# Performance work log

Hardware: AMD Instinct MI355X
Metric: run time of the kernel (lower is better)

## Reference

```python
import jax, jax.numpy as jnp
import numpy as np

B, N, C, H = 2, 2048, 768, 12
HD = C // H  # head dim = 64


def setup_inputs() -> dict:
    key = jax.random.key(0)
    k1, k2, k3 = jax.random.split(key, 3)
    x = jax.random.normal(k1, (B, N, C), dtype=jnp.float32)
    w_qkv = jax.random.normal(k2, (C, 3 * C), dtype=jnp.float32) * (C ** -0.5)
    w_proj = jax.random.normal(k3, (C, C), dtype=jnp.float32) * (C ** -0.5)
    b_proj = jnp.zeros((C,), dtype=jnp.float32)
    return {"x": x, "w_qkv": w_qkv, "w_proj": w_proj, "b_proj": b_proj}


def reference(x, w_qkv, w_proj, b_proj):
    scale = HD ** -0.5
    # qkv projection: [B,N,3C] -> [3,B,H,N,HD]
    qkv = (x @ w_qkv).reshape(B, N, 3, H, HD).transpose(2, 0, 3, 1, 4)
    q, k, v = qkv[0], qkv[1], qkv[2]
    # explicit QK^T softmax V (materializes [B,H,N,N] scores, as in source)
    attn = jnp.einsum("bhqd,bhkd->bhqk", q, k) * scale
    attn = jax.nn.softmax(attn, axis=-1)
    out = jnp.einsum("bhqk,bhkd->bhqd", attn, v)
    out = out.transpose(0, 2, 1, 3).reshape(B, N, C)
    return out @ w_proj + b_proj
```

## Files before the change

kernel.cpp:

```cpp
#include <hip/hip_runtime.h>

#define C_DIM 768
#define NSEQ 2048
#define H_DIM 12
#define HD 64
#define M_ROWS 4096
#define KSPLIT 4

typedef float f32x4 __attribute__((ext_vector_type(4)));
typedef short bf16x8 __attribute__((ext_vector_type(8)));
typedef _Float16 f16x8 __attribute__((ext_vector_type(8)));
typedef _Float16 f16x4 __attribute__((ext_vector_type(4)));
typedef __fp16 fp16x2 __attribute__((ext_vector_type(2)));
typedef __fp16 fp16x4 __attribute__((ext_vector_type(4)));
typedef unsigned short u16;

#define MFMA_PV(a, b, c) __builtin_amdgcn_mfma_f32_16x16x16f16(a, b, c, 0, 0, 0)

typedef unsigned int __attribute__((address_space(1))) as1_uint;
typedef unsigned int __attribute__((address_space(3))) as3_uint;
__device__ __forceinline__ void dma16(const void* g, void* l) {
  __builtin_amdgcn_global_load_lds((const as1_uint*)g, (as3_uint*)l, 16, 0, 0);
}

__device__ __forceinline__ u16 f2bf(float f) {
  union { float f; unsigned u; } v; v.f = f;
  unsigned u = v.u + 0x7FFFu + ((v.u >> 16) & 1u);
  return (u16)(u >> 16);
}

__global__ __launch_bounds__(256) void prep_kernel(const float* __restrict__ x,
                                                   const float* __restrict__ wq,
                                                   const float* __restrict__ wp,
                                                   u16* __restrict__ x_bf,
                                                   u16* __restrict__ outq,
                                                   u16* __restrict__ outp) {
  if (blockIdx.z == 2) {
    const int n4 = M_ROWS * C_DIM / 4;
    int lb = blockIdx.y * 72 + blockIdx.x;
    int i0 = lb * 256 + threadIdx.x;
    {
      float4 v = ((const float4*)x)[i0];
      ushort4 o;
      o.x = f2bf(v.x); o.y = f2bf(v.y); o.z = f2bf(v.z); o.w = f2bf(v.w);
      ((ushort4*)x_bf)[i0] = o;
    }
    int i1 = i0 + 442368;
    if (i1 < n4) {
      float4 v = ((const float4*)x)[i1];
      ushort4 o;
      o.x = f2bf(v.x); o.y = f2bf(v.y); o.z = f2bf(v.z); o.w = f2bf(v.w);
      ((ushort4*)x_bf)[i1] = o;
    }
    return;
  }
  const float* in; u16* out; int Cc;
  if (blockIdx.z == 0) { in = wq; out = outq; Cc = 3 * C_DIM; }
  else { if (blockIdx.x >= 24) return; in = wp; out = outp; Cc = C_DIM; }
  const int R = C_DIM;
  __shared__ float t[32][33];
  int tx = threadIdx.x & 31, ty = threadIdx.x >> 5;
  int c0 = blockIdx.x * 32, r0 = blockIdx.y * 32;
#pragma unroll
  for (int i = 0; i < 4; i++)
    t[ty + i * 8][tx] = in[(size_t)(r0 + ty + i * 8) * Cc + c0 + tx];
  __syncthreads();
#pragma unroll
  for (int i = 0; i < 4; i++)
    out[(size_t)(c0 + ty + i * 8) * R + r0 + tx] = f2bf(t[tx][ty + i * 8]);
}

__device__ __forceinline__ void gemm_core_128(const u16* __restrict__ A,
                                              const u16* __restrict__ BT,
                                              int m0, int n0,
                                              u16* la, u16* lb, f32x4 acc[4][4]) {
  const int K = C_DIM;
  int tid = threadIdx.x, lane = tid & 63, wave = tid >> 6;
  int wm = (wave >> 1) * 64, wn = (wave & 1) * 64;
  int quad = lane >> 4, l16 = lane & 15;

  int r0 = wave * 16 + (lane >> 2);
  int sw = (((lane & 3) ^ (r0 & 3)) * 8);
  const u16* ga0 = A + (size_t)(m0 + r0) * K + sw;
  const u16* ga1 = A + (size_t)(m0 + r0 + 64) * K + sw;
  const u16* gb0 = BT + (size_t)(n0 + r0) * K + sw;
  const u16* gb1 = BT + (size_t)(n0 + r0 + 64) * K + sw;
  u16* lA0 = la + wave * 16 * 32;
  u16* lA1 = lA0 + 64 * 32;
  u16* lB0 = lb + wave * 16 * 32;
  u16* lB1 = lB0 + 64 * 32;

  for (int k0 = 0; k0 < K; k0 += 32) {
    __syncthreads();
    dma16(ga0 + k0, lA0);
    dma16(ga1 + k0, lA1);
    dma16(gb0 + k0, lB0);
    dma16(gb1 + k0, lB1);
    __syncthreads();
    bf16x8 af[4], bfr[4];
#pragma unroll
    for (int mt = 0; mt < 4; mt++) {
      int r = wm + mt * 16 + l16;
      af[mt] = *(const bf16x8*)(la + r * 32 + ((quad ^ (r & 3)) * 8));
    }
#pragma unroll
    for (int nt = 0; nt < 4; nt++) {
      int r = wn + nt * 16 + l16;
      bfr[nt] = *(const bf16x8*)(lb + r * 32 + ((quad ^ (r & 3)) * 8));
    }
#pragma unroll
    for (int mt = 0; mt < 4; mt++)
#pragma unroll
      for (int nt = 0; nt < 4; nt++)
        acc[mt][nt] = __builtin_amdgcn_mfma_f32_16x16x32_bf16(af[mt], bfr[nt], acc[mt][nt], 0, 0, 0);
  }
}

__device__ __forceinline__ void gemm_core_64(const u16* __restrict__ A,
                                             const u16* __restrict__ BT,
                                             int m0, int n0,
                                             u16* la, u16* lb, f32x4 acc[2][4]) {
  const int K = C_DIM;
  int tid = threadIdx.x, lane = tid & 63, wave = tid >> 6;
  int wm = (wave >> 1) * 32, wn = (wave & 1) * 64;
  int quad = lane >> 4, l16 = lane & 15;

  int r0 = wave * 16 + (lane >> 2);
  int sw = (((lane & 3) ^ (r0 & 3)) * 8);
  const u16* ga0 = A + (size_t)(m0 + r0) * K + sw;
  const u16* gb0 = BT + (size_t)(n0 + r0) * K + sw;
  const u16* gb1 = BT + (size_t)(n0 + r0 + 64) * K + sw;
  u16* lA0 = la + wave * 16 * 32;
  u16* lB0 = lb + wave * 16 * 32;
  u16* lB1 = lB0 + 64 * 32;

  for (int k0 = 0; k0 < K; k0 += 32) {
    __syncthreads();
    dma16(ga0 + k0, lA0);
    dma16(gb0 + k0, lB0);
    dma16(gb1 + k0, lB1);
    __syncthreads();
    bf16x8 af[2], bfr[4];
#pragma unroll
    for (int mt = 0; mt < 2; mt++) {
      int r = wm + mt * 16 + l16;
      af[mt] = *(const bf16x8*)(la + r * 32 + ((quad ^ (r & 3)) * 8));
    }
#pragma unroll
    for (int nt = 0; nt < 4; nt++) {
      int r = wn + nt * 16 + l16;
      bfr[nt] = *(const bf16x8*)(lb + r * 32 + ((quad ^ (r & 3)) * 8));
    }
#pragma unroll
    for (int mt = 0; mt < 2; mt++)
#pragma unroll
      for (int nt = 0; nt < 4; nt++)
        acc[mt][nt] = __builtin_amdgcn_mfma_f32_16x16x32_bf16(af[mt], bfr[nt], acc[mt][nt], 0, 0, 0);
  }
}

#define Q_PRESCALE 0.18033688011112042f
__global__ __launch_bounds__(256) void gemm_qkv_kernel(const u16* __restrict__ A,
                                                       const u16* __restrict__ BT,
                                                       _Float16* __restrict__ qb,
                                                       _Float16* __restrict__ kb,
                                                       _Float16* __restrict__ vtb) {
  __shared__ __align__(16) u16 la[128 * 32];
  __shared__ __align__(16) u16 lb[128 * 32];
  f32x4 acc[4][4] = {};
  int m0 = blockIdx.x * 128, n0 = blockIdx.y * 128;
  gemm_core_128(A, BT, m0, n0, la, lb, acc);

  int lane = threadIdx.x & 63, wave = threadIdx.x >> 6;
  int wm = (wave >> 1) * 64, wn = (wave & 1) * 64;
  int quad = lane >> 4, l16 = lane & 15;
#pragma unroll
  for (int mt = 0; mt < 4; mt++) {
#pragma unroll
    for (int nt = 0; nt < 4; nt++) {
      int gn = n0 + wn + nt * 16 + l16;
      int which = gn / C_DIM;
      int cc = gn - which * C_DIM;
      int h = cc >> 6, d = cc & 63;
      int gm0 = m0 + wm + mt * 16 + quad * 4;
      int b = gm0 >> 11, n = gm0 & 2047;
      size_t bh = (size_t)(b * H_DIM + h);
      if (which == 2) {
        f16x4 hv;
#pragma unroll
        for (int r = 0; r < 4; r++) hv[r] = (_Float16)acc[mt][nt][r];
        *(f16x4*)(vtb + (bh * HD + d) * NSEQ + n) = hv;
      } else if (which == 0) {
#pragma unroll
        for (int r = 0; r < 4; r++)
          qb[(bh * NSEQ + n + r) * HD + d] = (_Float16)(acc[mt][nt][r] * Q_PRESCALE);
      } else {
#pragma unroll
        for (int r = 0; r < 4; r++)
          kb[(bh * NSEQ + n + r) * HD + d] = (_Float16)acc[mt][nt][r];
      }
    }
  }
}

__global__ __launch_bounds__(256) void gemm_proj_kernel(const u16* __restrict__ A,
                                                        const u16* __restrict__ BT,
                                                        const float* __restrict__ bias,
                                                        float* __restrict__ out) {
  __shared__ __align__(16) u16 la[64 * 32];
  __shared__ __align__(16) u16 lb[128 * 32];
  f32x4 acc[2][4] = {};
  int m0 = blockIdx.x * 64, n0 = blockIdx.y * 128;
  gemm_core_64(A, BT, m0, n0, la, lb, acc);

  int lane = threadIdx.x & 63, wave = threadIdx.x >> 6;
  int wm = (wave >> 1) * 32, wn = (wave & 1) * 64;
  int quad = lane >> 4, l16 = lane & 15;
#pragma unroll
  for (int mt = 0; mt < 2; mt++) {
#pragma unroll
    for (int nt = 0; nt < 4; nt++) {
      int gn = n0 + wn + nt * 16 + l16;
      float bv = bias[gn];
#pragma unroll
      for (int r = 0; r < 4; r++) {
        int gm = m0 + wm + mt * 16 + quad * 4 + r;
        out[(size_t)gm * C_DIM + gn] = acc[mt][nt][r] + bv;
      }
    }
  }
}

__global__ __launch_bounds__(256) void attn_kernel(const _Float16* __restrict__ qb,
                                                   const _Float16* __restrict__ kb,
                                                   const _Float16* __restrict__ vtb,
                                                   __fp16* __restrict__ opart,
                                                   float* __restrict__ lpart) {
  __shared__ __align__(16) u16 lk[2][64 * 72];
  __shared__ __align__(16) u16 lv[2][64 * 72];
  int bh = blockIdx.y, qblk = blockIdx.x, ks = blockIdx.z;
  int tid = threadIdx.x, lane = tid & 63, wave = tid >> 6;
  int quad = lane >> 4, l16 = lane & 15;

  const _Float16* q_bh = qb + (size_t)bh * NSEQ * HD;
  const u16* k_bh = (const u16*)(kb + (size_t)bh * NSEQ * HD);
  const u16* v_bh = (const u16*)(vtb + (size_t)bh * HD * NSEQ);

  int q0 = qblk * 128 + wave * 32 + l16;
  f16x8 qf[2][2];
#pragma unroll
  for (int qt = 0; qt < 2; qt++) {
    const _Float16* qp = q_bh + (size_t)(q0 + qt * 16) * HD + quad * 8;
    qf[qt][0] = *(const f16x8*)qp;
    qf[qt][1] = *(const f16x8*)(qp + 32);
  }

  f32x4 o[2][4] = {};
  float l_i[2] = {0.f, 0.f};

  int srow = tid >> 3, scj = tid & 7;
  const u16* kp0 = k_bh + (size_t)srow * HD + scj * 8;
  const u16* kp1 = kp0 + (size_t)32 * HD;
  const u16* vp0 = v_bh + (size_t)srow * NSEQ + scj * 8;
  const u16* vp1 = vp0 + (size_t)32 * NSEQ;
  int w0 = srow * 72 + scj * 8, w1 = (srow + 32) * 72 + scj * 8;

  const int kt_beg = ks * (NSEQ / 64 / KSPLIT);
  const int kt_end = kt_beg + (NSEQ / 64 / KSPLIT);

  {
    int k0 = kt_beg * 64;
    *(uint4*)(lk[0] + w0) = *(const uint4*)(kp0 + (size_t)k0 * HD);
    *(uint4*)(lk[0] + w1) = *(const uint4*)(kp1 + (size_t)k0 * HD);
    *(uint4*)(lv[0] + w0) = *(const uint4*)(vp0 + k0);
    *(uint4*)(lv[0] + w1) = *(const uint4*)(vp1 + k0);
  }

  for (int kt = kt_beg; kt < kt_end; kt++) {
    int cur = kt & 1, nxt = cur ^ 1;
    __syncthreads();

    uint4 rk0, rk1, rv0, rv1;
    if (kt < kt_end - 1) {
      int k0 = (kt + 1) * 64;
      rk0 = *(const uint4*)(kp0 + (size_t)k0 * HD);
      rk1 = *(const uint4*)(kp1 + (size_t)k0 * HD);
      rv0 = *(const uint4*)(vp0 + k0);
      rv1 = *(const uint4*)(vp1 + k0);
    }

    f32x4 s0[4], s1[4];
#pragma unroll
    for (int nt = 0; nt < 4; nt++) {
      const u16* kp = lk[cur] + (nt * 16 + l16) * 72 + quad * 8;
      f16x8 kf0 = *(const f16x8*)kp;
      f16x8 kf1 = *(const f16x8*)(kp + 32);
      f32x4 t0 = {}, t1 = {};
      t0 = __builtin_amdgcn_mfma_f32_16x16x32_f16(kf0, qf[0][0], t0, 0, 0, 0);
      t0 = __builtin_amdgcn_mfma_f32_16x16x32_f16(kf1, qf[0][1], t0, 0, 0, 0);
      t1 = __builtin_amdgcn_mfma_f32_16x16x32_f16(kf0, qf[1][0], t1, 0, 0, 0);
      t1 = __builtin_amdgcn_mfma_f32_16x16x32_f16(kf1, qf[1][1], t1, 0, 0, 0);
      s0[nt] = t0; s1[nt] = t1;
    }

#pragma unroll
    for (int nt = 0; nt < 4; nt++) {
      float a0 = __builtin_amdgcn_exp2f(s0[nt][0]);
      float a1 = __builtin_amdgcn_exp2f(s0[nt][1]);
      float a2 = __builtin_amdgcn_exp2f(s0[nt][2]);
      float a3 = __builtin_amdgcn_exp2f(s0[nt][3]);
      l_i[0] += (a0 + a1) + (a2 + a3);
      float b0 = __builtin_amdgcn_exp2f(s1[nt][0]);
      float b1 = __builtin_amdgcn_exp2f(s1[nt][1]);
      float b2 = __builtin_amdgcn_exp2f(s1[nt][2]);
      float b3 = __builtin_amdgcn_exp2f(s1[nt][3]);
      l_i[1] += (b0 + b1) + (b2 + b3);
      union { fp16x2 h2[2]; f16x4 h4; } pa, pb;
      pa.h2[0] = __builtin_amdgcn_cvt_pkrtz(a0, a1);
      pa.h2[1] = __builtin_amdgcn_cvt_pkrtz(a2, a3);
      pb.h2[0] = __builtin_amdgcn_cvt_pkrtz(b0, b1);
      pb.h2[1] = __builtin_amdgcn_cvt_pkrtz(b2, b3);
#pragma unroll
      for (int dt = 0; dt < 4; dt++) {
        f16x4 vf = *(const f16x4*)(lv[cur] + (dt * 16 + l16) * 72 + nt * 16 + quad * 4);
        o[0][dt] = MFMA_PV(vf, pa.h4, o[0][dt]);
        o[1][dt] = MFMA_PV(vf, pb.h4, o[1][dt]);
      }
    }

    if (kt < kt_end - 1) {
      *(uint4*)(lk[nxt] + w0) = rk0;
      *(uint4*)(lk[nxt] + w1) = rk1;
      *(uint4*)(lv[nxt] + w0) = rv0;
      *(uint4*)(lv[nxt] + w1) = rv1;
    }
  }

#pragma unroll
  for (int qt = 0; qt < 2; qt++) {
    l_i[qt] += __shfl_xor(l_i[qt], 16);
    l_i[qt] += __shfl_xor(l_i[qt], 32);
  }

  int b = bh / H_DIM, h = bh % H_DIM;
  __fp16* obase = opart + (size_t)ks * M_ROWS * C_DIM;
  float* lrow = lpart + ((size_t)ks * H_DIM * 2 + bh) * NSEQ;
#pragma unroll
  for (int qt = 0; qt < 2; qt++) {
    int q = q0 + qt * 16;
    if (quad == 0) lrow[q] = l_i[qt];
    __fp16* orow = obase + (size_t)(b * NSEQ + q) * C_DIM + h * HD;
#pragma unroll
    for (int dt = 0; dt < 4; dt++) {
      union { fp16x2 h2[2]; fp16x4 h4; } ov;
      ov.h2[0] = __builtin_amdgcn_cvt_pkrtz(o[qt][dt][0], o[qt][dt][1]);
      ov.h2[1] = __builtin_amdgcn_cvt_pkrtz(o[qt][dt][2], o[qt][dt][3]);
      *(fp16x4*)(orow + dt * 16 + quad * 4) = ov.h4;
    }
  }
}

__global__ __launch_bounds__(256) void combine_kernel(const __fp16* __restrict__ opart,
                                                      const float* __restrict__ lpart,
                                                      u16* __restrict__ attn) {
  int idx = blockIdx.x * 256 + threadIdx.x;
  int bq = idx / (C_DIM / 8);
  int c = (idx - bq * (C_DIM / 8)) * 8;
  int h = c >> 6;
  int b = bq >> 11, q = bq & 2047;
  float l = 0.f;
  float acc[8] = {0.f, 0.f, 0.f, 0.f, 0.f, 0.f, 0.f, 0.f};
  const __fp16* p = opart + (size_t)bq * C_DIM + c;
#pragma unroll
  for (int ks = 0; ks < KSPLIT; ks++) {
    l += lpart[((size_t)ks * H_DIM * 2 + b * H_DIM + h) * NSEQ + q];
    fp16x4 a0 = *(const fp16x4*)(p + (size_t)ks * M_ROWS * C_DIM);
    fp16x4 a1 = *(const fp16x4*)(p + (size_t)ks * M_ROWS * C_DIM + 4);
#pragma unroll
    for (int j = 0; j < 4; j++) { acc[j] += (float)a0[j]; acc[4 + j] += (float)a1[j]; }
  }
  float inv = 1.f / l;
  union { ushort4 s4[2]; uint4 u4; } ov;
  ov.s4[0].x = f2bf(acc[0] * inv);
  ov.s4[0].y = f2bf(acc[1] * inv);
  ov.s4[0].z = f2bf(acc[2] * inv);
  ov.s4[0].w = f2bf(acc[3] * inv);
  ov.s4[1].x = f2bf(acc[4] * inv);
  ov.s4[1].y = f2bf(acc[5] * inv);
  ov.s4[1].z = f2bf(acc[6] * inv);
  ov.s4[1].w = f2bf(acc[7] * inv);
  *(uint4*)(attn + (size_t)bq * C_DIM + c) = ov.u4;
}

extern "C" void kernel_launch(void* const* d_in, const int* in_sizes, int n_in,
                              void* d_out, int out_size, void* d_ws, size_t ws_size,
                              hipStream_t stream) {
  const float* x = (const float*)d_in[0];
  const float* w_qkv = (const float*)d_in[1];
  const float* w_proj = (const float*)d_in[2];
  const float* b_proj = (const float*)d_in[3];
  float* out = (float*)d_out;

  char* ws = (char*)d_ws;
  u16* x_bf        = (u16*)(ws);
  u16* wqkvT       = (u16*)(ws + 6291456);
  u16* wprojT      = (u16*)(ws + 9830400);
  _Float16* qb     = (_Float16*)(ws + 11010048);
  _Float16* kb     = (_Float16*)(ws + 17301504);
  _Float16* vtb    = (_Float16*)(ws + 23592960);
  __fp16* opart    = (__fp16*)(ws + 29884416);
  float* lpart     = (float*)(ws + 55050240);
  u16* attn        = x_bf;

  prep_kernel<<<dim3(72, 24, 3), 256, 0, stream>>>(x, w_qkv, w_proj, x_bf, wqkvT, wprojT);
  gemm_qkv_kernel<<<dim3(32, 18), 256, 0, stream>>>(x_bf, wqkvT, qb, kb, vtb);
  attn_kernel<<<dim3(16, 24, KSPLIT), 256, 0, stream>>>(qb, kb, vtb, opart, lpart);
  combine_kernel<<<M_ROWS * C_DIM / 8 / 256, 256, 0, stream>>>(opart, lpart, attn);
  gemm_proj_kernel<<<dim3(64, 6), 256, 0, stream>>>(attn, wprojT, b_proj, out);
}
```

Before: 161.2 us.

## Fuse split-KV combine into projection GEMM, halve KSPLIT, double-buffer GEMM LDS

```diff
diff --git a/kernel.cpp b/kernel.cpp
--- a/kernel.cpp
+++ b/kernel.cpp
@@ -5,7 +5,7 @@
 #define H_DIM 12
 #define HD 64
 #define M_ROWS 4096
-#define KSPLIT 4
+#define KSPLIT 2
 
 typedef float f32x4 __attribute__((ext_vector_type(4)));
 typedef short bf16x8 __attribute__((ext_vector_type(8)));
@@ -13,6 +13,7 @@
 typedef _Float16 f16x4 __attribute__((ext_vector_type(4)));
 typedef __fp16 fp16x2 __attribute__((ext_vector_type(2)));
 typedef __fp16 fp16x4 __attribute__((ext_vector_type(4)));
+typedef __fp16 fp16x8 __attribute__((ext_vector_type(8)));
 typedef unsigned short u16;
 
 #define MFMA_PV(a, b, c) __builtin_amdgcn_mfma_f32_16x16x16f16(a, b, c, 0, 0, 0)
@@ -34,7 +35,7 @@
                                                    const float* __restrict__ wp,
                                                    u16* __restrict__ x_bf,
                                                    u16* __restrict__ outq,
-                                                   u16* __restrict__ outp) {
+                                                   __fp16* __restrict__ outp) {
   if (blockIdx.z == 2) {
     const int n4 = M_ROWS * C_DIM / 4;
     int lb = blockIdx.y * 72 + blockIdx.x;
@@ -54,26 +55,37 @@
     }
     return;
   }
-  const float* in; u16* out; int Cc;
-  if (blockIdx.z == 0) { in = wq; out = outq; Cc = 3 * C_DIM; }
-  else { if (blockIdx.x >= 24) return; in = wp; out = outp; Cc = C_DIM; }
   const int R = C_DIM;
   __shared__ float t[32][33];
   int tx = threadIdx.x & 31, ty = threadIdx.x >> 5;
   int c0 = blockIdx.x * 32, r0 = blockIdx.y * 32;
-#pragma unroll
-  for (int i = 0; i < 4; i++)
-    t[ty + i * 8][tx] = in[(size_t)(r0 + ty + i * 8) * Cc + c0 + tx];
-  __syncthreads();
-#pragma unroll
-  for (int i = 0; i < 4; i++)
-    out[(size_t)(c0 + ty + i * 8) * R + r0 + tx] = f2bf(t[tx][ty + i * 8]);
-}
-
-__device__ __forceinline__ void gemm_core_128(const u16* __restrict__ A,
-                                              const u16* __restrict__ BT,
-                                              int m0, int n0,
-                                              u16* la, u16* lb, f32x4 acc[4][4]) {
+  if (blockIdx.z == 0) {
+    const int Cc = 3 * C_DIM;
+#pragma unroll
+    for (int i = 0; i < 4; i++)
+      t[ty + i * 8][tx] = wq[(size_t)(r0 + ty + i * 8) * Cc + c0 + tx];
+    __syncthreads();
+#pragma unroll
+    for (int i = 0; i < 4; i++)
+      outq[(size_t)(c0 + ty + i * 8) * R + r0 + tx] = f2bf(t[tx][ty + i * 8]);
+  } else {
+    if (blockIdx.x >= 24) return;
+    const int Cc = C_DIM;
+#pragma unroll
+    for (int i = 0; i < 4; i++)
+      t[ty + i * 8][tx] = wp[(size_t)(r0 + ty + i * 8) * Cc + c0 + tx];
+    __syncthreads();
+#pragma unroll
+    for (int i = 0; i < 4; i++)
+      outp[(size_t)(c0 + ty + i * 8) * R + r0 + tx] = (__fp16)t[tx][ty + i * 8];
+  }
+}
+
+__device__ __forceinline__ void gemm_core_128_db(const u16* __restrict__ A,
+                                                 const u16* __restrict__ BT,
+                                                 int m0, int n0,
+                                                 u16 (*la)[128 * 32], u16 (*lb)[128 * 32],
+                                                 f32x4 acc[4][4]) {
   const int K = C_DIM;
   int tid = threadIdx.x, lane = tid & 63, wave = tid >> 6;
   int wm = (wave >> 1) * 64, wn = (wave & 1) * 64;
@@ -85,74 +97,37 @@
   const u16* ga1 = A + (size_t)(m0 + r0 + 64) * K + sw;
   const u16* gb0 = BT + (size_t)(n0 + r0) * K + sw;
   const u16* gb1 = BT + (size_t)(n0 + r0 + 64) * K + sw;
-  u16* lA0 = la + wave * 16 * 32;
-  u16* lA1 = lA0 + 64 * 32;
-  u16* lB0 = lb + wave * 16 * 32;
-  u16* lB1 = lB0 + 64 * 32;
-
-  for (int k0 = 0; k0 < K; k0 += 32) {
+  int ofs0 = wave * 16 * 32, ofs1 = ofs0 + 64 * 32;
+
+  dma16(ga0, la[0] + ofs0);
+  dma16(ga1, la[0] + ofs1);
+  dma16(gb0, lb[0] + ofs0);
+  dma16(gb1, lb[0] + ofs1);
+
+  const int NT = K / 32;
+  for (int kt = 0; kt < NT; kt++) {
+    int cur = kt & 1, nxt = cur ^ 1;
     __syncthreads();
-    dma16(ga0 + k0, lA0);
-    dma16(ga1 + k0, lA1);
-    dma16(gb0 + k0, lB0);
-    dma16(gb1 + k0, lB1);
-    __syncthreads();
+    if (kt < NT - 1) {
+      int k0 = (kt + 1) * 32;
+      dma16(ga0 + k0, la[nxt] + ofs0);
+      dma16(ga1 + k0, la[nxt] + ofs1);
+      dma16(gb0 + k0, lb[nxt] + ofs0);
+      dma16(gb1 + k0, lb[nxt] + ofs1);
+    }
     bf16x8 af[4], bfr[4];
 #pragma unroll
     for (int mt = 0; mt < 4; mt++) {
       int r = wm + mt * 16 + l16;
-      af[mt] = *(const bf16x8*)(la + r * 32 + ((quad ^ (r & 3)) * 8));
+      af[mt] = *(const bf16x8*)(la[cur] + r * 32 + ((quad ^ (r & 3)) * 8));
     }
 #pragma unroll
     for (int nt = 0; nt < 4; nt++) {
       int r = wn + nt * 16 + l16;
-      bfr[nt] = *(const bf16x8*)(lb + r * 32 + ((quad ^ (r & 3)) * 8));
+      bfr[nt] = *(const bf16x8*)(lb[cur] + r * 32 + ((quad ^ (r & 3)) * 8));
     }
 #pragma unroll
     for (int mt = 0; mt < 4; mt++)
-#pragma unroll
-      for (int nt = 0; nt < 4; nt++)
-        acc[mt][nt] = __builtin_amdgcn_mfma_f32_16x16x32_bf16(af[mt], bfr[nt], acc[mt][nt], 0, 0, 0);
-  }
-}
-
-__device__ __forceinline__ void gemm_core_64(const u16* __restrict__ A,
-                                             const u16* __restrict__ BT,
-                                             int m0, int n0,
-                                             u16* la, u16* lb, f32x4 acc[2][4]) {
-  const int K = C_DIM;
-  int tid = threadIdx.x, lane = tid & 63, wave = tid >> 6;
-  int wm = (wave >> 1) * 32, wn = (wave & 1) * 64;
-  int quad = lane >> 4, l16 = lane & 15;
-
-  int r0 = wave * 16 + (lane >> 2);
-  int sw = (((lane & 3) ^ (r0 & 3)) * 8);
-  const u16* ga0 = A + (size_t)(m0 + r0) * K + sw;
-  const u16* gb0 = BT + (size_t)(n0 + r0) * K + sw;
-  const u16* gb1 = BT + (size_t)(n0 + r0 + 64) * K + sw;
-  u16* lA0 = la + wave * 16 * 32;
-  u16* lB0 = lb + wave * 16 * 32;
-  u16* lB1 = lB0 + 64 * 32;
-
-  for (int k0 = 0; k0 < K; k0 += 32) {
-    __syncthreads();
-    dma16(ga0 + k0, lA0);
-    dma16(gb0 + k0, lB0);
-    dma16(gb1 + k0, lB1);
-    __syncthreads();
-    bf16x8 af[2], bfr[4];
-#pragma unroll
-    for (int mt = 0; mt < 2; mt++) {
-      int r = wm + mt * 16 + l16;
-      af[mt] = *(const bf16x8*)(la + r * 32 + ((quad ^ (r & 3)) * 8));
-    }
-#pragma unroll
-    for (int nt = 0; nt < 4; nt++) {
-      int r = wn + nt * 16 + l16;
-      bfr[nt] = *(const bf16x8*)(lb + r * 32 + ((quad ^ (r & 3)) * 8));
-    }
-#pragma unroll
-    for (int mt = 0; mt < 2; mt++)
 #pragma unroll
       for (int nt = 0; nt < 4; nt++)
         acc[mt][nt] = __builtin_amdgcn_mfma_f32_16x16x32_bf16(af[mt], bfr[nt], acc[mt][nt], 0, 0, 0);
@@ -165,11 +140,11 @@
                                                        _Float16* __restrict__ qb,
                                                        _Float16* __restrict__ kb,
                                                        _Float16* __restrict__ vtb) {
-  __shared__ __align__(16) u16 la[128 * 32];
-  __shared__ __align__(16) u16 lb[128 * 32];
+  __shared__ __align__(16) u16 la[2][128 * 32];
+  __shared__ __align__(16) u16 lb[2][128 * 32];
   f32x4 acc[4][4] = {};
   int m0 = blockIdx.x * 128, n0 = blockIdx.y * 128;
-  gemm_core_128(A, BT, m0, n0, la, lb, acc);
+  gemm_core_128_db(A, BT, m0, n0, la, lb, acc);
 
   int lane = threadIdx.x & 63, wave = threadIdx.x >> 6;
   int wm = (wave >> 1) * 64, wn = (wave & 1) * 64;
@@ -203,19 +178,94 @@
   }
 }
 
-__global__ __launch_bounds__(256) void gemm_proj_kernel(const u16* __restrict__ A,
+__global__ __launch_bounds__(256) void gemm_proj_kernel(const __fp16* __restrict__ opart,
+                                                        const float* __restrict__ lpart,
                                                         const u16* __restrict__ BT,
                                                         const float* __restrict__ bias,
                                                         float* __restrict__ out) {
-  __shared__ __align__(16) u16 la[64 * 32];
-  __shared__ __align__(16) u16 lb[128 * 32];
+  __shared__ __align__(16) u16 la[2][64 * 32];
+  __shared__ __align__(16) u16 lb[2][128 * 32];
+  int tid = threadIdx.x, lane = tid & 63, wave = tid >> 6;
+  int quad = lane >> 4, l16 = lane & 15;
+  int wm = (wave >> 1) * 32, wn = (wave & 1) * 64;
+  int m0 = blockIdx.x * 64, n0 = blockIdx.y * 128;
+
+  int r0 = wave * 16 + (lane >> 2);
+  int swb = (((lane & 3) ^ (r0 & 3)) * 8);
+  const u16* gb0 = BT + (size_t)(n0 + r0) * C_DIM + swb;
+  const u16* gb1 = BT + (size_t)(n0 + r0 + 64) * C_DIM + swb;
+  int ofsB0 = wave * 16 * 32, ofsB1 = ofsB0 + 64 * 32;
+
+  int ar = r0, cj = lane & 3;
+  int m = m0 + ar;
+  int bb = m >> 11, q = m & 2047;
+  const __fp16* ap0 = opart + (size_t)m * C_DIM + cj * 8;
+  const __fp16* ap1 = ap0 + (size_t)M_ROWS * C_DIM;
+  int wslotA = ar * 32 + ((cj ^ (ar & 3)) * 8);
+
   f32x4 acc[2][4] = {};
-  int m0 = blockIdx.x * 64, n0 = blockIdx.y * 128;
-  gemm_core_64(A, BT, m0, n0, la, lb, acc);
-
-  int lane = threadIdx.x & 63, wave = threadIdx.x >> 6;
-  int wm = (wave >> 1) * 32, wn = (wave & 1) * 64;
-  int quad = lane >> 4, l16 = lane & 15;
+
+  union pk_t { fp16x2 h2[4]; uint4 v; };
+
+  dma16(gb0, lb[0] + ofsB0);
+  dma16(gb1, lb[0] + ofsB1);
+  {
+    fp16x8 p0 = *(const fp16x8*)ap0;
+    fp16x8 p1 = *(const fp16x8*)ap1;
+    float l = lpart[((size_t)bb * H_DIM + 0) * NSEQ + q] +
+              lpart[((size_t)(H_DIM * 2 + bb * H_DIM + 0)) * NSEQ + q];
+    float inv = 1.f / l;
+    pk_t w;
+#pragma unroll
+    for (int j = 0; j < 4; j++)
+      w.h2[j] = __builtin_amdgcn_cvt_pkrtz(((float)p0[2 * j] + (float)p1[2 * j]) * inv,
+                                           ((float)p0[2 * j + 1] + (float)p1[2 * j + 1]) * inv);
+    *(uint4*)(la[0] + wslotA) = w.v;
+  }
+
+  const int NT = C_DIM / 32;
+  for (int kt = 0; kt < NT; kt++) {
+    int cur = kt & 1, nxt = cur ^ 1;
+    __syncthreads();
+    fp16x8 p0, p1;
+    float inv = 0.f;
+    if (kt < NT - 1) {
+      int k0 = (kt + 1) * 32;
+      dma16(gb0 + k0, lb[nxt] + ofsB0);
+      dma16(gb1 + k0, lb[nxt] + ofsB1);
+      p0 = *(const fp16x8*)(ap0 + k0);
+      p1 = *(const fp16x8*)(ap1 + k0);
+      int h = (kt + 1) >> 1;
+      float l = lpart[((size_t)bb * H_DIM + h) * NSEQ + q] +
+                lpart[((size_t)(H_DIM * 2 + bb * H_DIM + h)) * NSEQ + q];
+      inv = 1.f / l;
+    }
+    f16x8 af[2], bf[4];
+#pragma unroll
+    for (int mt = 0; mt < 2; mt++) {
+      int r = wm + mt * 16 + l16;
+      af[mt] = *(const f16x8*)(la[cur] + r * 32 + ((quad ^ (r & 3)) * 8));
+    }
+#pragma unroll
+    for (int nt = 0; nt < 4; nt++) {
+      int r = wn + nt * 16 + l16;
+      bf[nt] = *(const f16x8*)(lb[cur] + r * 32 + ((quad ^ (r & 3)) * 8));
+    }
+#pragma unroll
+    for (int mt = 0; mt < 2; mt++)
+#pragma unroll
+      for (int nt = 0; nt < 4; nt++)
+        acc[mt][nt] = __builtin_amdgcn_mfma_f32_16x16x32_f16(af[mt], bf[nt], acc[mt][nt], 0, 0, 0);
+    if (kt < NT - 1) {
+      pk_t w;
+#pragma unroll
+      for (int j = 0; j < 4; j++)
+        w.h2[j] = __builtin_amdgcn_cvt_pkrtz(((float)p0[2 * j] + (float)p1[2 * j]) * inv,
+                                             ((float)p0[2 * j + 1] + (float)p1[2 * j + 1]) * inv);
+      *(uint4*)(la[nxt] + wslotA) = w.v;
+    }
+  }
+
 #pragma unroll
   for (int mt = 0; mt < 2; mt++) {
 #pragma unroll
@@ -360,38 +410,6 @@
   }
 }
 
-__global__ __launch_bounds__(256) void combine_kernel(const __fp16* __restrict__ opart,
-                                                      const float* __restrict__ lpart,
-                                                      u16* __restrict__ attn) {
-  int idx = blockIdx.x * 256 + threadIdx.x;
-  int bq = idx / (C_DIM / 8);
-  int c = (idx - bq * (C_DIM / 8)) * 8;
-  int h = c >> 6;
-  int b = bq >> 11, q = bq & 2047;
-  float l = 0.f;
-  float acc[8] = {0.f, 0.f, 0.f, 0.f, 0.f, 0.f, 0.f, 0.f};
-  const __fp16* p = opart + (size_t)bq * C_DIM + c;
-#pragma unroll
-  for (int ks = 0; ks < KSPLIT; ks++) {
-    l += lpart[((size_t)ks * H_DIM * 2 + b * H_DIM + h) * NSEQ + q];
-    fp16x4 a0 = *(const fp16x4*)(p + (size_t)ks * M_ROWS * C_DIM);
-    fp16x4 a1 = *(const fp16x4*)(p + (size_t)ks * M_ROWS * C_DIM + 4);
-#pragma unroll
-    for (int j = 0; j < 4; j++) { acc[j] += (float)a0[j]; acc[4 + j] += (float)a1[j]; }
-  }
-  float inv = 1.f / l;
-  union { ushort4 s4[2]; uint4 u4; } ov;
-  ov.s4[0].x = f2bf(acc[0] * inv);
-  ov.s4[0].y = f2bf(acc[1] * inv);
-  ov.s4[0].z = f2bf(acc[2] * inv);
-  ov.s4[0].w = f2bf(acc[3] * inv);
-  ov.s4[1].x = f2bf(acc[4] * inv);
-  ov.s4[1].y = f2bf(acc[5] * inv);
-  ov.s4[1].z = f2bf(acc[6] * inv);
-  ov.s4[1].w = f2bf(acc[7] * inv);
-  *(uint4*)(attn + (size_t)bq * C_DIM + c) = ov.u4;
-}
-
 extern "C" void kernel_launch(void* const* d_in, const int* in_sizes, int n_in,
                               void* d_out, int out_size, void* d_ws, size_t ws_size,
                               hipStream_t stream) {
@@ -404,17 +422,16 @@
   char* ws = (char*)d_ws;
   u16* x_bf        = (u16*)(ws);
   u16* wqkvT       = (u16*)(ws + 6291456);
-  u16* wprojT      = (u16*)(ws + 9830400);
+  __fp16* wprojT   = (__fp16*)(ws + 9830400);
   _Float16* qb     = (_Float16*)(ws + 11010048);
   _Float16* kb     = (_Float16*)(ws + 17301504);
   _Float16* vtb    = (_Float16*)(ws + 23592960);
   __fp16* opart    = (__fp16*)(ws + 29884416);
-  float* lpart     = (float*)(ws + 55050240);
-  u16* attn        = x_bf;
+  float* lpart     = (float*)(ws + 42467328);
 
   prep_kernel<<<dim3(72, 24, 3), 256, 0, stream>>>(x, w_qkv, w_proj, x_bf, wqkvT, wprojT);
   gemm_qkv_kernel<<<dim3(32, 18), 256, 0, stream>>>(x_bf, wqkvT, qb, kb, vtb);
   attn_kernel<<<dim3(16, 24, KSPLIT), 256, 0, stream>>>(qb, kb, vtb, opart, lpart);
-  combine_kernel<<<M_ROWS * C_DIM / 8 / 256, 256, 0, stream>>>(opart, lpart, attn);
-  gemm_proj_kernel<<<dim3(64, 6), 256, 0, stream>>>(attn, wprojT, b_proj, out);
-}
+  gemm_proj_kernel<<<dim3(64, 6), 256, 0, stream>>>(opart, lpart, (const u16*)wprojT,
+                                                    b_proj, out);
+}
```

Result: no change. 162.1 us (+0.6%).
